# Kernel tuning notes

Hardware: AMD Instinct MI355X
Metric: run time of the kernel (lower is better)

The kernel has to match this reference:

```python
import jax, jax.numpy as jnp
import numpy as np

EPS = 1e-5
L = 19        # number of semantic labels (fc_mu0..fc_mu18)
S = 512       # style_length


def conv3x3(x, w, b):
    # x: [B,C,H,W], w: [O,I,3,3] (torch OIHW), b: [O]
    y = jax.lax.conv_general_dilated(
        x, w, window_strides=(1, 1), padding='SAME',
        dimension_numbers=('NCHW', 'OIHW', 'NCHW'))
    return y + b[None, :, None, None]


def setup_inputs() -> dict:
    key = jax.random.key(0)
    ks = jax.random.split(key, 20)
    B, FIN, H, W = 4, 128, 256, 256
    inp = {
        'x': jax.random.normal(ks[0], (B, FIN, H, W), jnp.float32),
        'labels': jax.random.randint(ks[1], (B, H, W), 0, L),
        'noise': jax.random.normal(ks[2], (B, W, H, 1), jnp.float32),
        'style_codes': jax.random.normal(ks[3], (B, L, S), jnp.float32),
        # params
        'noise_var': 0.02 * jax.random.normal(ks[4], (FIN,), jnp.float32),
        'w_sh': 0.02 * jax.random.normal(ks[5], (128, L, 3, 3), jnp.float32),
        'b_sh': jnp.zeros((128,), jnp.float32),
        'w_g': 0.02 * jax.random.normal(ks[6], (FIN, 128, 3, 3), jnp.float32),
        'b_g': jnp.zeros((FIN,), jnp.float32),
        'w_b': 0.02 * jax.random.normal(ks[7], (FIN, 128, 3, 3), jnp.float32),
        'b_b': jnp.zeros((FIN,), jnp.float32),
        'Wfc': 0.02 * jax.random.normal(ks[8], (L, S, S), jnp.float32),  # [label, out, in]
        'bfc': jnp.zeros((L, S), jnp.float32),
        'w_cg': 0.02 * jax.random.normal(ks[9], (FIN, S, 3, 3), jnp.float32),
        'b_cg': jnp.zeros((FIN,), jnp.float32),
        'w_cb': 0.02 * jax.random.normal(ks[10], (FIN, S, 3, 3), jnp.float32),
        'b_cb': jnp.zeros((FIN,), jnp.float32),
        'g_blend': jnp.zeros((1,), jnp.float32),
        'b_blend': jnp.zeros((1,), jnp.float32),
    }
    return inp


def reference(x, labels, noise, style_codes, noise_var, w_sh, b_sh, w_g, b_g,
              w_b, b_b, Wfc, bfc, w_cg, b_cg, w_cb, b_cb, g_blend, b_blend):
    B, FIN, H, W = x.shape
    # added_noise: randn([B,W,H,1]) * noise_var[FIN] then transpose(1,3) -> [B,FIN,H,W]
    added = jnp.transpose(noise * noise_var, (0, 3, 2, 1))
    xn = x + added
    # param-free BatchNorm2d (training-mode batch stats, biased var)
    mean = jnp.mean(xn, axis=(0, 2, 3), keepdims=True)
    var = jnp.mean(jnp.square(xn - mean), axis=(0, 2, 3), keepdims=True)
    normalized = (xn - mean) / jnp.sqrt(var + EPS)

    # one-hot segmap [B,L,H,W]; interpolation to x's size is identity here
    seg = jnp.transpose(jax.nn.one_hot(labels, L, dtype=x.dtype), (0, 3, 1, 2))

    # per-label style FC: mu[b,j,:] = relu(fc_mu_j(style_codes[b,j]))
    mu = jax.nn.relu(jnp.einsum('bjd,jod->bjo', style_codes, Wfc) + bfc)  # [B,L,S]
    # masked_scatter with one-hot masks == per-pixel gather of the label's style code
    middle = mu[jnp.arange(B)[:, None, None], labels]        # [B,H,W,S]
    middle = jnp.transpose(middle, (0, 3, 1, 2))              # [B,S,H,W]

    gamma_avg = conv3x3(middle, w_cg, b_cg)
    beta_avg = conv3x3(middle, w_cb, b_cb)

    actv = jax.nn.relu(conv3x3(seg, w_sh, b_sh))
    gamma_spade = conv3x3(actv, w_g, b_g)
    beta_spade = conv3x3(actv, w_b, b_b)

    ga = jax.nn.sigmoid(g_blend)
    ba = jax.nn.sigmoid(b_blend)
    gamma_final = ga * gamma_avg + (1.0 - ga) * gamma_spade
    beta_final = ba * beta_avg + (1.0 - ba) * beta_spade
    return normalized * (1.0 + gamma_final) + beta_final
```

## Files before the change

kernel.cpp:

```cpp
#include <hip/hip_runtime.h>
#include <hip/hip_bf16.h>

#define NB   4
#define FIN  128
#define HH   256
#define WWW  256
#define LLAB 19
#define SSTY 512
#define HW   (HH*WWW)
#define NRED (NB*HW)

#define WS_NT   0
#define WS_SUM  262144
#define WS_SSQ  262272
#define WS_MEAN 262400
#define WS_ISTD 262528
#define WS_MU   262656
#define WS_A2   301568
#define WS_BSTG_B 1906688
#define WS_WSH_B  4855808

typedef __attribute__((ext_vector_type(8))) short bf16x8;
typedef __attribute__((ext_vector_type(4))) float f32x4;

__device__ inline unsigned short f2bf(float f) {
  __hip_bfloat16 h = __float2bfloat16(f);
  union { __hip_bfloat16 h; unsigned short u; } cv; cv.h = h; return cv.u;
}
__device__ inline float bf2f(short u) {
  union { unsigned int u; float f; } cv;
  cv.u = ((unsigned int)(unsigned short)u) << 16; return cv.f;
}

__device__ inline void gload_lds16(const void* g, void* l) {
  __builtin_amdgcn_global_load_lds(
      (const __attribute__((address_space(1))) void*)g,
      (__attribute__((address_space(3))) void*)l, 16, 0, 0);
}

__global__ __launch_bounds__(256) void kprep1(const float* __restrict__ noise,
                                              const float* __restrict__ style,
                                              const float* __restrict__ Wfc,
                                              const float* __restrict__ bfc,
                                              float* __restrict__ ws) {
  const int t = threadIdx.x;
  if (blockIdx.x < 256) {
    __shared__ float tile[32][33];
    int blk = blockIdx.x;
    int b = blk >> 6, by = (blk >> 3) & 7, bx = blk & 7;
    int w0 = bx * 32, h0 = by * 32;
    int txx = t & 31, tyy = t >> 5;
    #pragma unroll
    for (int j = 0; j < 4; ++j) {
      int wi = w0 + tyy + j * 8;
      tile[tyy + j * 8][txx] = noise[(size_t)(b * 256 + wi) * 256 + h0 + txx];
    }
    __syncthreads();
    #pragma unroll
    for (int j = 0; j < 4; ++j) {
      int hi = h0 + tyy + j * 8;
      ws[WS_NT + (size_t)(b * 256 + hi) * 256 + w0 + txx] = tile[txx][tyy + j * 8];
    }
  } else {
    int m = blockIdx.x - 256;
    int j = m >> 3, r = m & 7, b = r >> 1, half = r & 1;
    int o = half * 256 + t;
    const float4* wrow = (const float4*)(Wfc + ((size_t)j * 512 + o) * 512);
    const float4* srow = (const float4*)(style + ((size_t)b * 19 + j) * 512);
    float acc = 0.f;
    for (int d = 0; d < 128; ++d) {
      float4 w = wrow[d];
      float4 s = srow[d];
      acc = fmaf(w.x, s.x, acc); acc = fmaf(w.y, s.y, acc);
      acc = fmaf(w.z, s.z, acc); acc = fmaf(w.w, s.w, acc);
    }
    acc += bfc[j * 512 + o];
    ws[WS_MU + ((size_t)b * 19 + j) * 512 + o] = fmaxf(acc, 0.f);
  }
}

__global__ __launch_bounds__(512) void kprep2(const float* __restrict__ x,
                                              const float* __restrict__ nv,
                                              const float* __restrict__ w_cg,
                                              const float* __restrict__ w_cb,
                                              float* __restrict__ ws) {
  const int t = threadIdx.x;
  if (blockIdx.x < 512) {
    const int bc = blockIdx.x;
    const int b = bc >> 7, c = bc & 127;
    const float4* xp = (const float4*)(x + (size_t)bc * HW);
    const float4* np = (const float4*)(ws + WS_NT + (size_t)b * HW);
    const float nvc = nv[c];
    float s1 = 0.f, s2 = 0.f;
    for (int i = 0; i < 32; ++i) {
      float4 xv = xp[i * 512 + t];
      float4 nz = np[i * 512 + t];
      float v0 = xv.x + nvc * nz.x; s1 += v0; s2 = fmaf(v0, v0, s2);
      float v1 = xv.y + nvc * nz.y; s1 += v1; s2 = fmaf(v1, v1, s2);
      float v2 = xv.z + nvc * nz.z; s1 += v2; s2 = fmaf(v2, v2, s2);
      float v3 = xv.w + nvc * nz.w; s1 += v3; s2 = fmaf(v3, v3, s2);
    }
    #pragma unroll
    for (int m = 32; m; m >>= 1) { s1 += __shfl_xor(s1, m); s2 += __shfl_xor(s2, m); }
    if ((t & 63) == 0) { atomicAdd(&ws[WS_SUM + c], s1); atomicAdd(&ws[WS_SSQ + c], s2); }
  } else {
    __shared__ float wlds[32 * 288];
    const int blkm = blockIdx.x - 512;
    const int cblk = blkm & 7, ssplit = (blkm >> 3) & 3, b = blkm >> 5;
    const int conv = t / 144, r = t % 144, cl = r / 9, k = r % 9;
    const int c = cblk * 16 + cl;
    const float* mu = ws + WS_MU;
    float acc[19];
    #pragma unroll
    for (int l = 0; l < 19; ++l) acc[l] = 0.f;

    for (int chunk = 0; chunk < 4; ++chunk) {
      const int s0 = ssplit * 128 + chunk * 32;
      for (int i = t; i < 9216; i += 512) {
        int kx = i % 9, q = i / 9, sl = q & 31, cc = q >> 5;
        int cv2 = cc >> 4, cl2 = cc & 15;
        const float* src = cv2 ? w_cb : w_cg;
        float v = src[((size_t)(cblk * 16 + cl2) * 512 + s0 + sl) * 9 + kx];
        wlds[sl * 288 + cv2 * 144 + cl2 * 9 + kx] = v;
      }
      __syncthreads();
      if (t < 288) {
        for (int sl = 0; sl < 32; ++sl) {
          float w = wlds[sl * 288 + t];
          int s = s0 + sl;
          #pragma unroll
          for (int l = 0; l < 19; ++l)
            acc[l] = fmaf(mu[((size_t)b * 19 + l) * 512 + s], w, acc[l]);
        }
      }
      __syncthreads();
    }
    if (t < 288) {
      #pragma unroll
      for (int l = 0; l < 19; ++l)
        atomicAdd(&ws[WS_A2 + (((size_t)b * 19 + l) * 9 + k) * 256 + conv * 128 + c], acc[l]);
    }
  }
}

__global__ __launch_bounds__(256) void kprep3(const float* __restrict__ w_g,
                                              const float* __restrict__ w_b,
                                              const float* __restrict__ w_sh,
                                              const float* __restrict__ g_blend,
                                              const float* __restrict__ b_blend,
                                              char* __restrict__ wsb,
                                              float* __restrict__ ws) {
  if (blockIdx.x < 144) {
    int tid = blockIdx.x * 256 + threadIdx.x;
    int lane = tid & 63, grp = tid >> 6;
    int s36 = grp % 36, nb = grp / 36;
    int kk = s36 >> 2, cb = s36 & 3;
    int n = nb * 16 + (lane & 15);
    int conv = n & 1, cout = n >> 1;
    float blend = conv ? b_blend[0] : g_blend[0];
    float scale = 1.f - 1.f / (1.f + __expf(-blend));
    const float* src = conv ? w_b : w_g;
    bf16x8 v;
    #pragma unroll
    for (int i = 0; i < 8; ++i) {
      int k = s36 * 32 + (lane >> 4) * 8 + i;
      int kki = k >> 7, cin = k & 127;
      v[i] = (short)f2bf(scale * src[((size_t)cout * 128 + cin) * 9 + kki]);
    }
    size_t slot = (size_t)(kk * 5 + cb) * 16384 + (size_t)(nb * 64 + lane) * 16;
    #pragma unroll
    for (int bb = 0; bb < 4; ++bb)
      *(bf16x8*)(wsb + WS_BSTG_B + (size_t)bb * 45 * 16384 + slot) = v;
  } else if (blockIdx.x < 234) {
    int tid = (blockIdx.x - 144) * 256 + threadIdx.x;
    if (blockIdx.x == 144 && threadIdx.x < 128) {
      int c = threadIdx.x;
      float mean = ws[WS_SUM + c] / (float)NRED;
      float var = ws[WS_SSQ + c] / (float)NRED - mean * mean;
      ws[WS_MEAN + c] = mean;
      ws[WS_ISTD + c] = 1.f / sqrtf(var + 1e-5f);
    }
    if (tid < 23040) {
      int l = tid / 1152, r = tid % 1152, k = r >> 7, cin = r & 127;
      float v = (l == 0) ? 0.f : w_sh[((size_t)cin * 19 + (l - 1)) * 9 + k];
      ((unsigned short*)(wsb + WS_WSH_B))[tid] = f2bf(v);
    }
  } else {
    int tid = (blockIdx.x - 234) * 256 + threadIdx.x;
    int lane = tid & 63, grp = tid >> 6;
    int kk = grp % 9, nb = (grp / 9) % 16, b = grp / 144;
    int n = nb * 16 + (lane & 15);
    int conv = n & 1, cout = n >> 1;
    float blend = conv ? b_blend[0] : g_blend[0];
    float scale = 1.f / (1.f + __expf(-blend));
    bf16x8 v;
    #pragma unroll
    for (int i = 0; i < 8; ++i) {
      int l = (lane >> 4) * 8 + i;
      float val = 0.f;
      if (l < 19)
        val = scale * ws[WS_A2 + (((size_t)b * 19 + l) * 9 + kk) * 256 + conv * 128 + cout];
      v[i] = (short)f2bf(val);
    }
    *(bf16x8*)(wsb + WS_BSTG_B + ((size_t)b * 45 + kk * 5 + 4) * 16384 +
               (size_t)(nb * 64 + lane) * 16) = v;
  }
}

__global__ __launch_bounds__(1024, 4) void k_main(
    const float* __restrict__ x, const int* __restrict__ labels,
    const float* __restrict__ b_sh,
    const float* __restrict__ b_g, const float* __restrict__ b_b,
    const float* __restrict__ b_cg, const float* __restrict__ b_cb,
    const float* __restrict__ noise_var,
    const float* __restrict__ g_blend, const float* __restrict__ b_blend,
    const float* __restrict__ ws, float* __restrict__ out) {
  extern __shared__ char smem[];
  int* labt = (int*)smem;
  char* actv = smem + 1600;
  char* ohA  = smem + 84544;
  float* gbias = (float*)(smem + 110464);
  float* bbias = gbias + 128; float* nvl = gbias + 256;
  float* meanl = gbias + 384; float* istdl = gbias + 512; float* bshl = gbias + 640;
  char* buf0 = smem + 113536;
  char* buf1 = smem + 113536 + 16384;

  const int t = threadIdx.x;
  const int b = blockIdx.z;
  const int y0 = blockIdx.y * 16, x0 = blockIdx.x * 16;
  const char* wsb = (const char*)ws;
  const char* wshp = wsb + WS_WSH_B;

  if (t < 128) {
    float ga = 1.f / (1.f + __expf(-g_blend[0]));
    float ba = 1.f / (1.f + __expf(-b_blend[0]));
    gbias[t] = ga * b_cg[t] + (1.f - ga) * b_g[t];
    bbias[t] = ba * b_cb[t] + (1.f - ba) * b_b[t];
    nvl[t] = noise_var[t];
    meanl[t] = ws[WS_MEAN + t];
    istdl[t] = ws[WS_ISTD + t];
    bshl[t] = b_sh[t];
  }
  if (t < 400) {
    int ly = t / 20, lx = t % 20;
    int gy = y0 - 2 + ly, gx = x0 - 2 + lx;
    int v = 0;
    if ((unsigned)gy < 256u && (unsigned)gx < 256u)
      v = labels[((size_t)(b * 256 + gy)) * 256 + gx] + 1;
    labt[t] = v;
  }
  for (int i = t; i < 6480; i += 1024) ((unsigned int*)ohA)[i] = 0u;
  __syncthreads();

  for (int it = t; it < 5184; it += 1024) {
    int hp = it >> 4, cg = it & 15;
    int py = hp / 18, px = hp - py * 18;
    int gy = y0 - 1 + py, gx = x0 - 1 + px;
    int baddr = hp * 256 + ((cg * 16) ^ ((hp & 15) << 4));
    bf16x8 o = {0, 0, 0, 0, 0, 0, 0, 0};
    if ((unsigned)gy < 256u && (unsigned)gx < 256u) {
      float accv[8];
      #pragma unroll
      for (int j = 0; j < 8; ++j) accv[j] = bshl[cg * 8 + j];
      #pragma unroll
      for (int k = 0; k < 9; ++k) {
        int dy = k / 3, dx = k - 3 * (k / 3);
        int lv = labt[(py + dy) * 20 + (px + dx)];
        bf16x8 wvv = *(const bf16x8*)(wshp + (size_t)((lv * 9 + k) * 128 + cg * 8) * 2);
        #pragma unroll
        for (int j = 0; j < 8; ++j) accv[j] += bf2f(wvv[j]);
      }
      #pragma unroll
      for (int j = 0; j < 8; ++j) o[j] = (short)f2bf(fmaxf(accv[j], 0.f));
    }
    *(bf16x8*)(actv + baddr) = o;
  }
  if (t < 324) {
    int py = t / 18, px = t - (t / 18) * 18;
    int gy = y0 - 1 + py, gx = x0 - 1 + px;
    if ((unsigned)gy < 256u && (unsigned)gx < 256u) {
      int lv = labt[(py + 1) * 20 + (px + 1)];
      ((unsigned short*)ohA)[t * 40 + (lv - 1)] = 0x3F80;
    }
  }
  __syncthreads();

  const int lane = t & 63;
  const int wid = t >> 6;
  const int wm = wid & 3, wn = wid >> 2;
  const int l15 = lane & 15, l16 = lane >> 4;
  const char* bsrc = wsb + WS_BSTG_B + (size_t)b * 45 * 16384 + (size_t)t * 16;
  const int bof = (wn * 4) * 1024 + lane * 16;

  f32x4 acc[4][4];
  #pragma unroll
  for (int i = 0; i < 4; ++i)
    #pragma unroll
    for (int j = 0; j < 4; ++j) acc[i][j] = (f32x4){0.f, 0.f, 0.f, 0.f};

#define PHASE(CB, KYV, KXV, CURBUF, DO_STAGE, STG_SRC, NXTBUF, VMC) { \
  if (DO_STAGE) gload_lds16(STG_SRC, NXTBUF + t * 16); \
  asm volatile("s_waitcnt vmcnt(%0)" :: "i"(VMC) : "memory"); \
  __builtin_amdgcn_s_barrier(); \
  __builtin_amdgcn_sched_barrier(0); \
  bf16x8 bfr_[4]; \
  _Pragma("unroll") \
  for (int nf_ = 0; nf_ < 4; ++nf_) \
    bfr_[nf_] = *(const bf16x8*)(CURBUF + bof + nf_ * 1024); \
  bf16x8 af_[4]; \
  _Pragma("unroll") \
  for (int mf_ = 0; mf_ < 4; ++mf_) { \
    int hp_ = (wm * 4 + mf_ + (KYV)) * 18 + l15 + (KXV); \
    if ((CB) < 4) \
      af_[mf_] = *(const bf16x8*)(actv + hp_ * 256 + (((CB) * 64 + l16 * 16) ^ ((hp_ & 15) << 4))); \
    else \
      af_[mf_] = *(const bf16x8*)(ohA + hp_ * 80 + l16 * 16); \
  } \
  __builtin_amdgcn_s_setprio(1); \
  _Pragma("unroll") \
  for (int mf_ = 0; mf_ < 4; ++mf_) \
    _Pragma("unroll") \
    for (int nf_ = 0; nf_ < 4; ++nf_) \
      acc[mf_][nf_] = __builtin_amdgcn_mfma_f32_16x16x32_bf16(af_[mf_], bfr_[nf_], acc[mf_][nf_], 0, 0, 0); \
  __builtin_amdgcn_s_setprio(0); \
  __builtin_amdgcn_sched_barrier(0); \
  __builtin_amdgcn_s_barrier(); }

  gload_lds16(bsrc, buf0 + t * 16);

  for (int q = 0; q < 4; ++q) {
    const int kk0 = 2 * q, kk1 = kk0 + 1;
    const int ky0 = kk0 / 3, kx0 = kk0 - 3 * ky0;
    const int ky1 = kk1 / 3, kx1 = kk1 - 3 * ky1;
    const char* bq = bsrc + (size_t)q * 10 * 16384;
    PHASE(0, ky0, kx0, buf0, true, bq + 1 * 16384, buf1, 1)
    PHASE(1, ky0, kx0, buf1, true, bq + 2 * 16384, buf0, 1)
    PHASE(2, ky0, kx0, buf0, true, bq + 3 * 16384, buf1, 1)
    PHASE(3, ky0, kx0, buf1, true, bq + 4 * 16384, buf0, 1)
    PHASE(4, ky0, kx0, buf0, true, bq + 5 * 16384, buf1, 1)
    PHASE(0, ky1, kx1, buf1, true, bq + 6 * 16384, buf0, 1)
    PHASE(1, ky1, kx1, buf0, true, bq + 7 * 16384, buf1, 1)
    PHASE(2, ky1, kx1, buf1, true, bq + 8 * 16384, buf0, 1)
    PHASE(3, ky1, kx1, buf0, true, bq + 9 * 16384, buf1, 1)
    PHASE(4, ky1, kx1, buf1, true, bq + 10 * 16384, buf0, 1)
  }
  {
    const char* bq = bsrc + (size_t)40 * 16384;
    PHASE(0, 2, 2, buf0, true, bq + 1 * 16384, buf1, 1)
    PHASE(1, 2, 2, buf1, true, bq + 2 * 16384, buf0, 1)
    PHASE(2, 2, 2, buf0, true, bq + 3 * 16384, buf1, 1)
    PHASE(3, 2, 2, buf1, true, bq + 4 * 16384, buf0, 1)
    PHASE(4, 2, 2, buf0, false, bq, buf1, 0)
  }
#undef PHASE

  const float* nt = ws + WS_NT + (size_t)b * HW;
  float* eps = (float*)(smem + 1600);

  #pragma unroll
  for (int chunk = 0; chunk < 4; ++chunk) {
    __syncthreads();
    #pragma unroll
    for (int mf = 0; mf < 4; ++mf) {
      int widx = (wn * 16 + l15) * 260 + (wm * 4 + mf) * 16 + l16 * 4;
      *(f32x4*)(eps + widx) = acc[mf][chunk];
    }
    __syncthreads();
    #pragma unroll
    for (int rep = 0; rep < 2; ++rep) {
      int u = rep * 1024 + t;
      int xq = u & 3, y = (u >> 2) & 15, ci = u >> 6;
      int wnp = ci >> 3, q = ci & 7;
      int c = wnp * 32 + chunk * 8 + q;
      int rg = wnp * 16 + 2 * q;
      f32x4 g4 = *(const f32x4*)(eps + rg * 260 + y * 16 + xq * 4);
      f32x4 b4 = *(const f32x4*)(eps + (rg + 1) * 260 + y * 16 + xq * 4);
      const float gb_ = gbias[c], bb_ = bbias[c];
      const float mn = meanl[c], is = istdl[c], nv = nvl[c];
      size_t off = (((size_t)(b * 128 + c)) * 256 + (y0 + y)) * 256 + x0 + xq * 4;
      float4 xv = *(const float4*)(x + off);
      float4 nz = *(const float4*)(nt + (y0 + y) * 256 + x0 + xq * 4);
      float4 o;
      o.x = ((xv.x + nv * nz.x) - mn) * is * (1.f + g4[0] + gb_) + (b4[0] + bb_);
      o.y = ((xv.y + nv * nz.y) - mn) * is * (1.f + g4[1] + gb_) + (b4[1] + bb_);
      o.z = ((xv.z + nv * nz.z) - mn) * is * (1.f + g4[2] + gb_) + (b4[2] + bb_);
      o.w = ((xv.w + nv * nz.w) - mn) * is * (1.f + g4[3] + gb_) + (b4[3] + bb_);
      *(float4*)(out + off) = o;
    }
  }
}

extern "C" void kernel_launch(void* const* d_in, const int* in_sizes, int n_in,
                              void* d_out, int out_size, void* d_ws, size_t ws_size,
                              hipStream_t stream) {
  const float* x        = (const float*)d_in[0];
  const int*   labels   = (const int*)d_in[1];
  const float* noise    = (const float*)d_in[2];
  const float* style    = (const float*)d_in[3];
  const float* nvar     = (const float*)d_in[4];
  const float* w_sh     = (const float*)d_in[5];
  const float* b_sh     = (const float*)d_in[6];
  const float* w_g      = (const float*)d_in[7];
  const float* b_g      = (const float*)d_in[8];
  const float* w_b      = (const float*)d_in[9];
  const float* b_b      = (const float*)d_in[10];
  const float* Wfc      = (const float*)d_in[11];
  const float* bfc      = (const float*)d_in[12];
  const float* w_cg     = (const float*)d_in[13];
  const float* b_cg     = (const float*)d_in[14];
  const float* w_cb     = (const float*)d_in[15];
  const float* b_cb     = (const float*)d_in[16];
  const float* g_blend  = (const float*)d_in[17];
  const float* b_blend  = (const float*)d_in[18];
  float* ws  = (float*)d_ws;
  char*  wsb = (char*)d_ws;
  float* out = (float*)d_out;

  static bool attr_set = false;
  if (!attr_set) {
    (void)hipFuncSetAttribute((const void*)k_main,
                              hipFuncAttributeMaxDynamicSharedMemorySize, 146304);
    attr_set = true;
  }

  hipMemsetAsync((char*)d_ws + (size_t)WS_SUM * 4, 0, 256 * 4, stream);
  hipMemsetAsync((char*)d_ws + (size_t)WS_A2 * 4, 0, (size_t)175104 * 4, stream);

  kprep1<<<dim3(408), dim3(256), 0, stream>>>(noise, style, Wfc, bfc, ws);
  kprep2<<<dim3(640), dim3(512), 0, stream>>>(x, nvar, w_cg, w_cb, ws);
  kprep3<<<dim3(378), dim3(256), 0, stream>>>(w_g, w_b, w_sh, g_blend, b_blend, wsb, ws);
  k_main<<<dim3(16, 16, 4), dim3(1024), 146304, stream>>>(
      x, labels, b_sh, b_g, b_b, b_cg, b_cb,
      nvar, g_blend, b_blend, ws, out);
}
```

Measured before the change: 303.2 us.

## Triple-buffer B staging with one barrier per phase and a tighter one-hot stride

The B-operand staging in LDS moves from a double buffer to a triple buffer. Each prefetch is issued after the barrier, two stages ahead, so the trailing barrier per MFMA phase can be removed. The loop is also restructured so each outer iteration covers one kernel row (ky) over three kx offsets. The one-hot A tile row stride shrinks from 80 to 72 bytes to help fit the extra buffer. Dynamic LDS grows to about 160KB, and the narrower 72-byte stride may change bank-conflict behaviour.

Measured after the change: 370.1 us. +22.1%, slower.

```diff
diff --git a/kernel.cpp b/kernel.cpp
--- a/kernel.cpp
+++ b/kernel.cpp
@@ -219,11 +219,10 @@
   int* labt = (int*)smem;
   char* actv = smem + 1600;
   char* ohA  = smem + 84544;
-  float* gbias = (float*)(smem + 110464);
+  float* gbias = (float*)(smem + 107872);
   float* bbias = gbias + 128; float* nvl = gbias + 256;
   float* meanl = gbias + 384; float* istdl = gbias + 512; float* bshl = gbias + 640;
-  char* buf0 = smem + 113536;
-  char* buf1 = smem + 113536 + 16384;
+  char* bstg = smem + 110944;
 
   const int t = threadIdx.x;
   const int b = blockIdx.z;
@@ -249,7 +248,7 @@
       v = labels[((size_t)(b * 256 + gy)) * 256 + gx] + 1;
     labt[t] = v;
   }
-  for (int i = t; i < 6480; i += 1024) ((unsigned int*)ohA)[i] = 0u;
+  for (int i = t; i < 5832; i += 1024) ((unsigned int*)ohA)[i] = 0u;
   __syncthreads();
 
   for (int it = t; it < 5184; it += 1024) {
@@ -280,7 +279,7 @@
     int gy = y0 - 1 + py, gx = x0 - 1 + px;
     if ((unsigned)gy < 256u && (unsigned)gx < 256u) {
       int lv = labt[(py + 1) * 20 + (px + 1)];
-      ((unsigned short*)ohA)[t * 40 + (lv - 1)] = 0x3F80;
+      ((unsigned short*)ohA)[t * 36 + (lv - 1)] = 0x3F80;
     }
   }
   __syncthreads();
@@ -291,6 +290,9 @@
   const int l15 = lane & 15, l16 = lane >> 4;
   const char* bsrc = wsb + WS_BSTG_B + (size_t)b * 45 * 16384 + (size_t)t * 16;
   const int bof = (wn * 4) * 1024 + lane * 16;
+  char* bufs0 = bstg;
+  char* bufs1 = bstg + 16384;
+  char* bufs2 = bstg + 32768;
 
   f32x4 acc[4][4];
   #pragma unroll
@@ -298,23 +300,23 @@
     #pragma unroll
     for (int j = 0; j < 4; ++j) acc[i][j] = (f32x4){0.f, 0.f, 0.f, 0.f};
 
-#define PHASE(CB, KYV, KXV, CURBUF, DO_STAGE, STG_SRC, NXTBUF, VMC) { \
-  if (DO_STAGE) gload_lds16(STG_SRC, NXTBUF + t * 16); \
+#define PHASE(CB, KXV, CUR, NXT, SLOC, DO_STAGE, VMC) { \
   asm volatile("s_waitcnt vmcnt(%0)" :: "i"(VMC) : "memory"); \
   __builtin_amdgcn_s_barrier(); \
   __builtin_amdgcn_sched_barrier(0); \
+  if (DO_STAGE) gload_lds16(bq + (size_t)((SLOC) + 2) * 16384, NXT + t * 16); \
   bf16x8 bfr_[4]; \
   _Pragma("unroll") \
   for (int nf_ = 0; nf_ < 4; ++nf_) \
-    bfr_[nf_] = *(const bf16x8*)(CURBUF + bof + nf_ * 1024); \
+    bfr_[nf_] = *(const bf16x8*)(CUR + bof + nf_ * 1024); \
   bf16x8 af_[4]; \
   _Pragma("unroll") \
   for (int mf_ = 0; mf_ < 4; ++mf_) { \
-    int hp_ = (wm * 4 + mf_ + (KYV)) * 18 + l15 + (KXV); \
+    int hp_ = (wm * 4 + mf_ + q) * 18 + l15 + (KXV); \
     if ((CB) < 4) \
       af_[mf_] = *(const bf16x8*)(actv + hp_ * 256 + (((CB) * 64 + l16 * 16) ^ ((hp_ & 15) << 4))); \
     else \
-      af_[mf_] = *(const bf16x8*)(ohA + hp_ * 80 + l16 * 16); \
+      af_[mf_] = *(const bf16x8*)(ohA + hp_ * 72 + l16 * 16); \
   } \
   __builtin_amdgcn_s_setprio(1); \
   _Pragma("unroll") \
@@ -322,35 +324,29 @@
     _Pragma("unroll") \
     for (int nf_ = 0; nf_ < 4; ++nf_) \
       acc[mf_][nf_] = __builtin_amdgcn_mfma_f32_16x16x32_bf16(af_[mf_], bfr_[nf_], acc[mf_][nf_], 0, 0, 0); \
-  __builtin_amdgcn_s_setprio(0); \
-  __builtin_amdgcn_sched_barrier(0); \
-  __builtin_amdgcn_s_barrier(); }
-
-  gload_lds16(bsrc, buf0 + t * 16);
-
-  for (int q = 0; q < 4; ++q) {
-    const int kk0 = 2 * q, kk1 = kk0 + 1;
-    const int ky0 = kk0 / 3, kx0 = kk0 - 3 * ky0;
-    const int ky1 = kk1 / 3, kx1 = kk1 - 3 * ky1;
-    const char* bq = bsrc + (size_t)q * 10 * 16384;
-    PHASE(0, ky0, kx0, buf0, true, bq + 1 * 16384, buf1, 1)
-    PHASE(1, ky0, kx0, buf1, true, bq + 2 * 16384, buf0, 1)
-    PHASE(2, ky0, kx0, buf0, true, bq + 3 * 16384, buf1, 1)
-    PHASE(3, ky0, kx0, buf1, true, bq + 4 * 16384, buf0, 1)
-    PHASE(4, ky0, kx0, buf0, true, bq + 5 * 16384, buf1, 1)
-    PHASE(0, ky1, kx1, buf1, true, bq + 6 * 16384, buf0, 1)
-    PHASE(1, ky1, kx1, buf0, true, bq + 7 * 16384, buf1, 1)
-    PHASE(2, ky1, kx1, buf1, true, bq + 8 * 16384, buf0, 1)
-    PHASE(3, ky1, kx1, buf0, true, bq + 9 * 16384, buf1, 1)
-    PHASE(4, ky1, kx1, buf1, true, bq + 10 * 16384, buf0, 1)
-  }
-  {
-    const char* bq = bsrc + (size_t)40 * 16384;
-    PHASE(0, 2, 2, buf0, true, bq + 1 * 16384, buf1, 1)
-    PHASE(1, 2, 2, buf1, true, bq + 2 * 16384, buf0, 1)
-    PHASE(2, 2, 2, buf0, true, bq + 3 * 16384, buf1, 1)
-    PHASE(3, 2, 2, buf1, true, bq + 4 * 16384, buf0, 1)
-    PHASE(4, 2, 2, buf0, false, bq, buf1, 0)
+  __builtin_amdgcn_s_setprio(0); }
+
+  gload_lds16(bsrc, bufs0 + t * 16);
+  gload_lds16(bsrc + 16384, bufs1 + t * 16);
+
+  for (int q = 0; q < 3; ++q) {
+    const char* bq = bsrc + (size_t)q * 15 * 16384;
+    const bool last = (q == 2);
+    PHASE(0, 0, bufs0, bufs2, 0, true, 1)
+    PHASE(1, 0, bufs1, bufs0, 1, true, 1)
+    PHASE(2, 0, bufs2, bufs1, 2, true, 1)
+    PHASE(3, 0, bufs0, bufs2, 3, true, 1)
+    PHASE(4, 0, bufs1, bufs0, 4, true, 1)
+    PHASE(0, 1, bufs2, bufs1, 5, true, 1)
+    PHASE(1, 1, bufs0, bufs2, 6, true, 1)
+    PHASE(2, 1, bufs1, bufs0, 7, true, 1)
+    PHASE(3, 1, bufs2, bufs1, 8, true, 1)
+    PHASE(4, 1, bufs0, bufs2, 9, true, 1)
+    PHASE(0, 2, bufs1, bufs0, 10, true, 1)
+    PHASE(1, 2, bufs2, bufs1, 11, true, 1)
+    PHASE(2, 2, bufs0, bufs2, 12, true, 1)
+    PHASE(3, 2, bufs1, bufs0, 13, !last, 1)
+    PHASE(4, 2, bufs2, bufs1, 14, !last, (last ? 0 : 1))
   }
 #undef PHASE
 
@@ -370,9 +366,9 @@
     for (int rep = 0; rep < 2; ++rep) {
       int u = rep * 1024 + t;
       int xq = u & 3, y = (u >> 2) & 15, ci = u >> 6;
-      int wnp = ci >> 3, q = ci & 7;
-      int c = wnp * 32 + chunk * 8 + q;
-      int rg = wnp * 16 + 2 * q;
+      int wnp = ci >> 3, qq = ci & 7;
+      int c = wnp * 32 + chunk * 8 + qq;
+      int rg = wnp * 16 + 2 * qq;
       f32x4 g4 = *(const f32x4*)(eps + rg * 260 + y * 16 + xq * 4);
       f32x4 b4 = *(const f32x4*)(eps + (rg + 1) * 260 + y * 16 + xq * 4);
       const float gb_ = gbias[c], bb_ = bbias[c];
@@ -419,7 +415,7 @@
   static bool attr_set = false;
   if (!attr_set) {
     (void)hipFuncSetAttribute((const void*)k_main,
-                              hipFuncAttributeMaxDynamicSharedMemorySize, 146304);
+                              hipFuncAttributeMaxDynamicSharedMemorySize, 160096);
     attr_set = true;
   }
 
@@ -429,7 +425,7 @@
   kprep1<<<dim3(408), dim3(256), 0, stream>>>(noise, style, Wfc, bfc, ws);
   kprep2<<<dim3(640), dim3(512), 0, stream>>>(x, nvar, w_cg, w_cb, ws);
   kprep3<<<dim3(378), dim3(256), 0, stream>>>(w_g, w_b, w_sh, g_blend, b_blend, wsb, ws);
-  k_main<<<dim3(16, 16, 4), dim3(1024), 146304, stream>>>(
+  k_main<<<dim3(16, 16, 4), dim3(1024), 160096, stream>>>(
       x, labels, b_sh, b_g, b_b, b_cg, b_cb,
       nvar, g_blend, b_blend, ws, out);
 }
```
